# Kernel tuning notes

Measured on AMD Instinct MI355X. Metric: run time of the kernel, lower is better.

Reference implementation:

```python
import jax, jax.numpy as jnp
import numpy as np

B, T, C = 2, 2048, 2048
H, D = 16, 128  # num_heads, head_dim


def setup_inputs() -> dict:
    key = jax.random.key(0)
    ks = jax.random.split(key, 5)
    x = jax.random.normal(ks[0], (B, T, C), dtype=jnp.float32)
    # causal mask: mask==0 positions are filled with -inf
    mask = jnp.tril(jnp.ones((T, T), dtype=jnp.int32))[None, None, :, :]
    wq = jax.random.normal(ks[1], (C, C), dtype=jnp.float32) * (C ** -0.5)
    wk = jax.random.normal(ks[2], (C, C), dtype=jnp.float32) * (C ** -0.5)
    wv = jax.random.normal(ks[3], (C, C), dtype=jnp.float32) * (C ** -0.5)
    wo = jax.random.normal(ks[4], (C, C), dtype=jnp.float32) * (C ** -0.5)
    return {"x": x, "mask": mask, "wq": wq, "wk": wk, "wv": wv, "wo": wo}


def reference(x, mask, wq, wk, wv, wo):
    Bx, Tx, Cx = x.shape
    scale = D ** -0.5
    # torch Linear: y = x @ W.T (weights are [out, in])
    q = (x @ wq.T).reshape(Bx, Tx, H, D).transpose(0, 2, 1, 3)  # [B,H,T,D]
    k = (x @ wk.T).reshape(Bx, Tx, H, D).transpose(0, 2, 1, 3)
    v = (x @ wv.T).reshape(Bx, Tx, H, D).transpose(0, 2, 1, 3)
    scores = jnp.einsum("bhqd,bhkd->bhqk", q, k) * scale  # [B,H,T,T]
    scores = jnp.where(mask == 0, -jnp.inf, scores)
    attn = jax.nn.softmax(scores, axis=-1)
    out = jnp.einsum("bhqk,bhkd->bhqd", attn, v)  # [B,H,T,D]
    out = out.transpose(0, 2, 1, 3).reshape(Bx, Tx, Cx)
    return out @ wo.T
```

## Files before the change

### kernel.cpp

```cpp
#include <hip/hip_runtime.h>
#include <hip/hip_bf16.h>


#define BB 2
#define TT 2048
#define CC 2048
#define HH 16
#define DD 128
#define MM (BB*TT)
#define NQT (TT/64)
#define GNT (CC/64)

typedef __bf16 bf16x8 __attribute__((ext_vector_type(8)));
typedef __bf16 bf16x4 __attribute__((ext_vector_type(4)));
typedef float  f32x4  __attribute__((ext_vector_type(4)));

#define MFMA16(a, b, c) __builtin_amdgcn_mfma_f32_16x16x32_bf16((a), (b), (c), 0, 0, 0)

__device__ __forceinline__ void g2lds16(const void* g, void* l) {
    __builtin_amdgcn_global_load_lds(
        (const __attribute__((address_space(1))) void*)g,
        (__attribute__((address_space(3))) void*)l,
        16, 0, 0);
}

__global__ __launch_bounds__(256) void cvt_all(
    const float* __restrict__ x,  const float* __restrict__ wq,
    const float* __restrict__ wk, const float* __restrict__ wv,
    const float* __restrict__ wo, __bf16* __restrict__ out_base)
{
    const int idx = blockIdx.x * 256 + threadIdx.x;
    const float* in; int off;
    if (idx < (1 << 21)) { in = x; off = idx; }
    else {
        const int r = idx - (1 << 21);
        const int k = r >> 20;
        in  = (k == 0) ? wq : (k == 1) ? wk : (k == 2) ? wv : wo;
        off = r & ((1 << 20) - 1);
    }
    const float4 v = ((const float4*)in)[off];
    bf16x4 o;
    o.x = (__bf16)v.x; o.y = (__bf16)v.y;
    o.z = (__bf16)v.z; o.w = (__bf16)v.w;
    ((bf16x4*)out_base)[idx] = o;
}

template<int MODE>
__global__ __launch_bounds__(512, 2) void gemm_bt(
    const __bf16* __restrict__ A, const __bf16* __restrict__ Wt,
    void* __restrict__ out)
{
    __shared__ __align__(16) __bf16 As[3][256*64];
    __shared__ __align__(16) __bf16 Bs[3][2][128*32];

    const int tid = threadIdx.x;
    const int w   = tid >> 6, lane = tid & 63;
    const int wm  = w >> 1,  wn  = w & 1;
    const int lo  = lane & 15, hi = lane >> 4;
    const int xr  = (lo & 7) << 4;
    const int xb2 = ((lo >> 1) & 3) << 4;

    const int bid   = blockIdx.y * gridDim.x + blockIdx.x;
    const int xcd   = bid & 7, loc = bid >> 3;
    const int n0    = (2*xcd + (loc & 1)) * 128;
    const int m0    = (loc >> 1) * 256;

    const int ar   = tid >> 3, as_ = tid & 7;
    const int acol = ((as_ ^ (ar & 7)) << 3);
    const int br   = tid >> 2, bs_ = tid & 3;
    const int bcol = ((bs_ ^ ((br >> 1) & 3)) << 3);

    auto stageA3a = [&](int buf, int kt) {
        #pragma unroll
        for (int j = 0; j < 3; ++j)
            g2lds16(A + (size_t)(m0 + j*64 + ar)*CC + kt*64 + acol,
                    (char*)&As[buf][0] + j*8192 + w*1024);
    };
    auto stageA3b = [&](int buf, int kt) {
        g2lds16(A + (size_t)(m0 + 3*64 + ar)*CC + kt*64 + acol,
                (char*)&As[buf][0] + 3*8192 + w*1024);
        #pragma unroll
        for (int kh = 0; kh < 2; ++kh)
            g2lds16(Wt + (size_t)(n0 + br)*CC + kt*64 + kh*32 + bcol,
                    (char*)&Bs[buf][kh][0] + w*1024);
    };
    auto rdA = [&](bf16x8* af, int buf, int ks) {
        const char* base = (const char*)&As[buf][0];
        #pragma unroll
        for (int mf = 0; mf < 4; ++mf) {
            const int r = wm*64 + mf*16 + lo;
            af[mf] = *(const bf16x8*)(base + r*128 + ((ks*64 + hi*16) ^ xr));
        }
    };
    auto rdB = [&](bf16x8* bv, int buf, int ks) {
        const char* base = (const char*)&Bs[buf][ks][0];
        #pragma unroll
        for (int nf = 0; nf < 4; ++nf) {
            const int n = wn*64 + nf*16 + lo;
            bv[nf] = *(const bf16x8*)(base + n*64 + ((hi*16) ^ xb2));
        }
    };

    f32x4 acc[4][4] = {};

    stageA3a(0, 0); stageA3b(0, 0);
    stageA3a(1, 1); stageA3b(1, 1);
    asm volatile("s_waitcnt vmcnt(6)" ::: "memory");
    __builtin_amdgcn_s_barrier();

    int rb = 0;
    #pragma unroll 1
    for (int t = 0; t < GNT - 2; ++t) {
        const int sb = (rb == 0) ? 2 : rb - 1;
        {
            bf16x8 af[4], bv[4];
            rdA(af, rb, 0); rdB(bv, rb, 0);
            stageA3a(sb, t + 2);
            __builtin_amdgcn_s_barrier();
            __builtin_amdgcn_s_setprio(1);
            #pragma unroll
            for (int mf = 0; mf < 4; ++mf)
                #pragma unroll
                for (int nf = 0; nf < 4; ++nf)
                    acc[mf][nf] = MFMA16(af[mf], bv[nf], acc[mf][nf]);
            __builtin_amdgcn_s_setprio(0);
            __builtin_amdgcn_s_barrier();
        }
        {
            bf16x8 af[4], bv[4];
            rdA(af, rb, 1); rdB(bv, rb, 1);
            stageA3b(sb, t + 2);
            __builtin_amdgcn_s_barrier();
            __builtin_amdgcn_s_setprio(1);
            #pragma unroll
            for (int mf = 0; mf < 4; ++mf)
                #pragma unroll
                for (int nf = 0; nf < 4; ++nf)
                    acc[mf][nf] = MFMA16(af[mf], bv[nf], acc[mf][nf]);
            __builtin_amdgcn_s_setprio(0);
            asm volatile("s_waitcnt vmcnt(6)" ::: "memory");
            __builtin_amdgcn_s_barrier();
        }
        rb = (rb == 2) ? 0 : rb + 1;
    }
    {
        bf16x8 af[4], bv[4];
        rdA(af, rb, 0); rdB(bv, rb, 0);
        __builtin_amdgcn_s_barrier();
        #pragma unroll
        for (int mf = 0; mf < 4; ++mf)
            #pragma unroll
            for (int nf = 0; nf < 4; ++nf)
                acc[mf][nf] = MFMA16(af[mf], bv[nf], acc[mf][nf]);
        __builtin_amdgcn_s_barrier();
        rdA(af, rb, 1); rdB(bv, rb, 1);
        #pragma unroll
        for (int mf = 0; mf < 4; ++mf)
            #pragma unroll
            for (int nf = 0; nf < 4; ++nf)
                acc[mf][nf] = MFMA16(af[mf], bv[nf], acc[mf][nf]);
        asm volatile("s_waitcnt vmcnt(0)" ::: "memory");
        __builtin_amdgcn_s_barrier();
        rb = (rb == 2) ? 0 : rb + 1;
    }
    {
        bf16x8 af[4], bv[4];
        rdA(af, rb, 0); rdB(bv, rb, 0);
        #pragma unroll
        for (int mf = 0; mf < 4; ++mf)
            #pragma unroll
            for (int nf = 0; nf < 4; ++nf)
                acc[mf][nf] = MFMA16(af[mf], bv[nf], acc[mf][nf]);
        rdA(af, rb, 1); rdB(bv, rb, 1);
        #pragma unroll
        for (int mf = 0; mf < 4; ++mf)
            #pragma unroll
            for (int nf = 0; nf < 4; ++nf)
                acc[mf][nf] = MFMA16(af[mf], bv[nf], acc[mf][nf]);
    }

    #pragma unroll
    for (int mf = 0; mf < 4; ++mf) {
        #pragma unroll
        for (int nf = 0; nf < 4; ++nf) {
            #pragma unroll
            for (int r = 0; r < 4; ++r) {
                const int row = m0 + wm*64 + mf*16 + hi*4 + r;
                const int col = n0 + wn*64 + nf*16 + lo;
                const float v = acc[mf][nf][r];
                if (MODE == 0) {
                    const int b = row >> 11, t = row & (TT-1);
                    const int h = col >> 7,  d = col & (DD-1);
                    ((__bf16*)out)[(size_t)((b*HH + h)*TT + t)*DD + d] = (__bf16)v;
                } else if (MODE == 1) {
                    const int b = row >> 11, t = row & (TT-1);
                    const int h = col >> 7,  d = col & (DD-1);
                    ((__bf16*)out)[(size_t)((b*HH + h)*DD + d)*TT + t] = (__bf16)v;
                } else {
                    ((float*)out)[(size_t)row*CC + col] = v;
                }
            }
        }
    }
}

__global__ __launch_bounds__(256, 2) void attn_fwd(
    const __bf16* __restrict__ Q, const __bf16* __restrict__ K,
    const __bf16* __restrict__ Vt, __bf16* __restrict__ O)
{
    __shared__ __align__(16) __bf16 Ks[2][64*128];
    __shared__ __align__(16) __bf16 Vs[2][128*64];
    __shared__ __align__(16) __bf16 Ps[4][16*64];

    const int lid   = blockIdx.y * gridDim.x + blockIdx.x;
    const int bh    = lid & 31;
    const int pairx = lid >> 5;
    const int tid = threadIdx.x;
    const int w   = tid >> 6, lane = tid & 63;
    const int lo  = lane & 15, hi = lane >> 4;
    const int xr  = (lo & 7) << 4;

    const int krow_l  = lane >> 4;
    const int kcol_sw = ((lane & 15) << 4);
    const int vrow_l  = lane >> 3;
    const int vcol_sw = (((lane & 7) ^ (lane >> 3)) << 3);

    const size_t kbase = (size_t)bh * TT * DD;
    const size_t vbase = (size_t)bh * DD * TT;
    const int b = bh >> 4, h = bh & 15;
    const float SC = 0.12754613142f;

    auto stage = [&](int buf, int kv0) {
        #pragma unroll
        for (int i = 0; i < 4; ++i) {
            const int c = 4*w + i;
            {
                const int row = 4*c + krow_l;
                const int sw  = (kcol_sw ^ ((row & 7) << 4)) >> 1;
                g2lds16(K + kbase + (size_t)(kv0 + row)*DD + sw,
                        &Ks[buf][0] + c*512);
            }
            {
                const int row = 8*c + vrow_l;
                g2lds16(Vt + vbase + (size_t)row*TT + kv0 + vcol_sw,
                        &Vs[buf][0] + c*512);
            }
        }
    };

    #pragma unroll 1
    for (int half = 0; half < 2; ++half) {
        const int qt = half ? pairx : (NQT - 1 - pairx);
        const int q0 = qt * 64;

        const __bf16* Qbase = Q + (kbase + (size_t)(q0 + w*16 + lo) * DD);
        bf16x8 qf[4];
        #pragma unroll
        for (int kc = 0; kc < 4; ++kc)
            qf[kc] = *(const bf16x8*)(Qbase + kc*32 + hi*8);

        float mrow[4], lrow[4];
        #pragma unroll
        for (int r = 0; r < 4; ++r) { mrow[r] = -1e30f; lrow[r] = 0.f; }
        f32x4 oacc[8] = {};

        const int qg_base = q0 + w*16 + hi*4;
        const int ntiles  = qt + 1;

        stage(0, 0);
        __syncthreads();
        int cur = 0;

        for (int t = 0; t < ntiles; ++t) {
            const int kv0 = t*64;
            if (t + 1 < ntiles) stage(cur ^ 1, (t+1)*64);

            const char* Kb = (const char*)&Ks[cur][0];
            const char* Vb = (const char*)&Vs[cur][0];

            f32x4 s[4];
            __builtin_amdgcn_s_setprio(1);
            #pragma unroll
            for (int st = 0; st < 4; ++st) {
                f32x4 a = {};
                #pragma unroll
                for (int kc = 0; kc < 4; ++kc) {
                    const bf16x8 kf = *(const bf16x8*)(
                        Kb + (st*16 + lo)*256 + ((kc*64 + hi*16) ^ xr));
                    a = MFMA16(qf[kc], kf, a);
                }
                s[st] = a;
            }
            __builtin_amdgcn_s_setprio(0);

            float pmax[4];
            const bool diag = (t == ntiles - 1);
            #pragma unroll
            for (int r = 0; r < 4; ++r) {
                const int qg = qg_base + r;
                float mx = -1e30f;
                #pragma unroll
                for (int st = 0; st < 4; ++st) {
                    float v = s[st][r] * SC;
                    if (diag) {
                        const int kvg = kv0 + st*16 + lo;
                        v = (kvg > qg) ? -1e30f : v;
                    }
                    s[st][r] = v;
                    mx = fmaxf(mx, v);
                }
                #pragma unroll
                for (int msk = 1; msk < 16; msk <<= 1)
                    mx = fmaxf(mx, __shfl_xor(mx, msk, 64));
                pmax[r] = mx;
            }

            bool need = false;
            #pragma unroll
            for (int r = 0; r < 4; ++r)
                need = need || (pmax[r] > mrow[r] + 11.5f);
            if (__any(need)) {
                float rsc[4];
                #pragma unroll
                for (int r = 0; r < 4; ++r) {
                    const float mnew = fmaxf(mrow[r], pmax[r]);
                    rsc[r]  = __builtin_amdgcn_exp2f(mrow[r] - mnew);
                    mrow[r] = mnew;
                    lrow[r] *= rsc[r];
                }
                #pragma unroll
                for (int dc = 0; dc < 8; ++dc)
                    #pragma unroll
                    for (int r = 0; r < 4; ++r)
                        oacc[dc][r] *= rsc[r];
            }

            float psum[4];
            #pragma unroll
            for (int r = 0; r < 4; ++r) {
                float ps = 0.f;
                #pragma unroll
                for (int st = 0; st < 4; ++st) {
                    const float pv = __builtin_amdgcn_exp2f(s[st][r] - mrow[r]);
                    s[st][r] = pv;
                    ps += pv;
                }
                psum[r] = ps;
            }
            #pragma unroll
            for (int r = 0; r < 4; ++r) {
                #pragma unroll
                for (int msk = 1; msk < 16; msk <<= 1)
                    psum[r] += __shfl_xor(psum[r], msk, 64);
                lrow[r] += psum[r];
            }

            char* Pw = (char*)&Ps[w][0];
            #pragma unroll
            for (int st = 0; st < 4; ++st)
                #pragma unroll
                for (int r = 0; r < 4; ++r) {
                    const int row = hi*4 + r;
                    *(__bf16*)(Pw + row*128 + (((st*16 + lo)*2) ^ ((row & 7) << 4)))
                        = (__bf16)s[st][r];
                }

            __builtin_amdgcn_s_setprio(1);
            #pragma unroll
            for (int kc2 = 0; kc2 < 2; ++kc2) {
                const bf16x8 pf = *(const bf16x8*)(
                    Pw + lo*128 + ((kc2*64 + hi*16) ^ xr));
                #pragma unroll
                for (int dc = 0; dc < 8; ++dc) {
                    const bf16x8 vf = *(const bf16x8*)(
                        Vb + (dc*16 + lo)*128 + ((kc2*64 + hi*16) ^ xr));
                    oacc[dc] = MFMA16(pf, vf, oacc[dc]);
                }
            }
            __builtin_amdgcn_s_setprio(0);

            __syncthreads();
            cur ^= 1;
        }

        #pragma unroll
        for (int r = 0; r < 4; ++r) {
            const float inv = 1.f / lrow[r];
            const int qg = qg_base + r;
            #pragma unroll
            for (int dc = 0; dc < 8; ++dc) {
                const int d = dc*16 + lo;
                O[(size_t)(b*TT + qg)*CC + h*DD + d] = (__bf16)(oacc[dc][r] * inv);
            }
        }
    }
}

extern "C" void kernel_launch(void* const* d_in, const int* in_sizes, int n_in,
                              void* d_out, int out_size, void* d_ws, size_t ws_size,
                              hipStream_t stream) {
    const float* x  = (const float*)d_in[0];
    const float* wq = (const float*)d_in[2];
    const float* wk = (const float*)d_in[3];
    const float* wv = (const float*)d_in[4];
    const float* wo = (const float*)d_in[5];

    char* p = (char*)d_ws;
    __bf16* xb  = (__bf16*)p; p += (size_t)MM*CC*2;
    __bf16* wqb = (__bf16*)p; p += (size_t)CC*CC*2;
    __bf16* wkb = (__bf16*)p; p += (size_t)CC*CC*2;
    __bf16* wvb = (__bf16*)p; p += (size_t)CC*CC*2;
    __bf16* wob = (__bf16*)p; p += (size_t)CC*CC*2;
    __bf16* Qb  = (__bf16*)p; p += (size_t)MM*CC*2;
    __bf16* Kb  = (__bf16*)p; p += (size_t)MM*CC*2;
    __bf16* Vtb = (__bf16*)p; p += (size_t)MM*CC*2;
    __bf16* AOb = xb;

    cvt_all<<<24576, 256, 0, stream>>>(x, wq, wk, wv, wo, xb);

    const dim3 gg(CC/128, MM/256);
    gemm_bt<0><<<gg, 512, 0, stream>>>(xb, wqb, Qb);
    gemm_bt<0><<<gg, 512, 0, stream>>>(xb, wkb, Kb);
    gemm_bt<1><<<gg, 512, 0, stream>>>(xb, wvb, Vtb);

    attn_fwd<<<dim3(NQT/2, BB*HH), 256, 0, stream>>>(Qb, Kb, Vtb, AOb);

    gemm_bt<2><<<gg, 512, 0, stream>>>(AOb, wob, (void*)d_out);
}
```

Baseline: 248.8 us.

## Halve attention KV tile to 32, raise occupancy, one query tile per block

```diff
diff --git a/kernel.cpp b/kernel.cpp
--- a/kernel.cpp
+++ b/kernel.cpp
@@ -10,6 +10,7 @@
 #define MM (BB*TT)
 #define NQT (TT/64)
 #define GNT (CC/64)
+#define KVB 32
 
 typedef __bf16 bf16x8 __attribute__((ext_vector_type(8)));
 typedef __bf16 bf16x4 __attribute__((ext_vector_type(4)));
@@ -204,26 +205,24 @@
     }
 }
 
-__global__ __launch_bounds__(256, 2) void attn_fwd(
+__global__ __launch_bounds__(256, 4) void attn_fwd(
     const __bf16* __restrict__ Q, const __bf16* __restrict__ K,
     const __bf16* __restrict__ Vt, __bf16* __restrict__ O)
 {
-    __shared__ __align__(16) __bf16 Ks[2][64*128];
-    __shared__ __align__(16) __bf16 Vs[2][128*64];
-    __shared__ __align__(16) __bf16 Ps[4][16*64];
-
-    const int lid   = blockIdx.y * gridDim.x + blockIdx.x;
-    const int bh    = lid & 31;
-    const int pairx = lid >> 5;
+    __shared__ __align__(16) __bf16 Ks[2][KVB*128];
+    __shared__ __align__(16) __bf16 Vs[2][128*KVB];
+    __shared__ __align__(16) __bf16 Ps[4][16*KVB];
+
+    const int bh = blockIdx.x;
+    const int aq = blockIdx.y & 7, bq = blockIdx.y >> 3;
+    const int qt = 8*bq + ((bq & 1) ? 7 - aq : aq);
+    const int q0 = qt * 64;
+
     const int tid = threadIdx.x;
     const int w   = tid >> 6, lane = tid & 63;
     const int lo  = lane & 15, hi = lane >> 4;
     const int xr  = (lo & 7) << 4;
-
-    const int krow_l  = lane >> 4;
-    const int kcol_sw = ((lane & 15) << 4);
-    const int vrow_l  = lane >> 3;
-    const int vcol_sw = (((lane & 7) ^ (lane >> 3)) << 3);
+    const int pvx = ((lo & 3) ^ ((lo >> 2) & 3)) << 4;
 
     const size_t kbase = (size_t)bh * TT * DD;
     const size_t vbase = (size_t)bh * DD * TT;
@@ -232,166 +231,161 @@
 
     auto stage = [&](int buf, int kv0) {
         #pragma unroll
-        for (int i = 0; i < 4; ++i) {
-            const int c = 4*w + i;
+        for (int i = 0; i < 2; ++i) {
+            const int c = 2*w + i;
             {
-                const int row = 4*c + krow_l;
-                const int sw  = (kcol_sw ^ ((row & 7) << 4)) >> 1;
+                const int row = 4*c + (lane >> 4);
+                const int sw  = ((((lane & 15) << 4) ^ ((row & 7) << 4)) >> 1);
                 g2lds16(K + kbase + (size_t)(kv0 + row)*DD + sw,
                         &Ks[buf][0] + c*512);
             }
             {
-                const int row = 8*c + vrow_l;
-                g2lds16(Vt + vbase + (size_t)row*TT + kv0 + vcol_sw,
+                const int rl  = lane >> 2;
+                const int row = 16*c + rl;
+                const int el  = ((((lane & 3) ^ (rl & 3) ^ ((rl >> 2) & 3))) << 3);
+                g2lds16(Vt + vbase + (size_t)row*TT + kv0 + el,
                         &Vs[buf][0] + c*512);
             }
         }
     };
 
-    #pragma unroll 1
-    for (int half = 0; half < 2; ++half) {
-        const int qt = half ? pairx : (NQT - 1 - pairx);
-        const int q0 = qt * 64;
-
-        const __bf16* Qbase = Q + (kbase + (size_t)(q0 + w*16 + lo) * DD);
-        bf16x8 qf[4];
-        #pragma unroll
-        for (int kc = 0; kc < 4; ++kc)
-            qf[kc] = *(const bf16x8*)(Qbase + kc*32 + hi*8);
-
-        float mrow[4], lrow[4];
-        #pragma unroll
-        for (int r = 0; r < 4; ++r) { mrow[r] = -1e30f; lrow[r] = 0.f; }
-        f32x4 oacc[8] = {};
-
-        const int qg_base = q0 + w*16 + hi*4;
-        const int ntiles  = qt + 1;
-
-        stage(0, 0);
+    const __bf16* Qbase = Q + (kbase + (size_t)(q0 + w*16 + lo) * DD);
+    bf16x8 qf[4];
+    #pragma unroll
+    for (int kc = 0; kc < 4; ++kc)
+        qf[kc] = *(const bf16x8*)(Qbase + kc*32 + hi*8);
+
+    float mrow[4], lrow[4];
+    #pragma unroll
+    for (int r = 0; r < 4; ++r) { mrow[r] = -1e30f; lrow[r] = 0.f; }
+    f32x4 oacc[8] = {};
+
+    const int qg_base = q0 + w*16 + hi*4;
+    const int ntiles  = 2*(qt + 1);
+
+    stage(0, 0);
+    __syncthreads();
+    int cur = 0;
+
+    for (int t = 0; t < ntiles; ++t) {
+        const int kv0 = t*KVB;
+        if (t + 1 < ntiles) stage(cur ^ 1, (t+1)*KVB);
+
+        const char* Kb = (const char*)&Ks[cur][0];
+        const char* Vb = (const char*)&Vs[cur][0];
+
+        f32x4 s[2];
+        __builtin_amdgcn_s_setprio(1);
+        #pragma unroll
+        for (int st = 0; st < 2; ++st) {
+            f32x4 a = {};
+            #pragma unroll
+            for (int kc = 0; kc < 4; ++kc) {
+                const bf16x8 kf = *(const bf16x8*)(
+                    Kb + (st*16 + lo)*256 + ((kc*64 + hi*16) ^ xr));
+                a = MFMA16(qf[kc], kf, a);
+            }
+            s[st] = a;
+        }
+        __builtin_amdgcn_s_setprio(0);
+
+        float pmax[4];
+        const bool diag = (t >= ntiles - 2);
+        #pragma unroll
+        for (int r = 0; r < 4; ++r) {
+            const int qg = qg_base + r;
+            float mx = -1e30f;
+            #pragma unroll
+            for (int st = 0; st < 2; ++st) {
+                float v = s[st][r] * SC;
+                if (diag) {
+                    const int kvg = kv0 + st*16 + lo;
+                    v = (kvg > qg) ? -1e30f : v;
+                }
+                s[st][r] = v;
+                mx = fmaxf(mx, v);
+            }
+            #pragma unroll
+            for (int msk = 1; msk < 16; msk <<= 1)
+                mx = fmaxf(mx, __shfl_xor(mx, msk, 64));
+            pmax[r] = mx;
+        }
+
+        bool need = false;
+        #pragma unroll
+        for (int r = 0; r < 4; ++r)
+            need = need || (pmax[r] > mrow[r] + 11.5f);
+        if (__any(need)) {
+            float rsc[4];
+            #pragma unroll
+            for (int r = 0; r < 4; ++r) {
+                const float mnew = fmaxf(mrow[r], pmax[r]);
+                rsc[r]  = __builtin_amdgcn_exp2f(mrow[r] - mnew);
+                mrow[r] = mnew;
+                lrow[r] *= rsc[r];
+            }
+            #pragma unroll
+            for (int dc = 0; dc < 8; ++dc)
+                #pragma unroll
+                for (int r = 0; r < 4; ++r)
+                    oacc[dc][r] *= rsc[r];
+        }
+
+        float psum[4];
+        #pragma unroll
+        for (int r = 0; r < 4; ++r) {
+            float ps = 0.f;
+            #pragma unroll
+            for (int st = 0; st < 2; ++st) {
+                const float pv = __builtin_amdgcn_exp2f(s[st][r] - mrow[r]);
+                s[st][r] = pv;
+                ps += pv;
+            }
+            psum[r] = ps;
+        }
+        #pragma unroll
+        for (int r = 0; r < 4; ++r) {
+            #pragma unroll
+            for (int msk = 1; msk < 16; msk <<= 1)
+                psum[r] += __shfl_xor(psum[r], msk, 64);
+            lrow[r] += psum[r];
+        }
+
+        char* Pw = (char*)&Ps[w][0];
+        #pragma unroll
+        for (int st = 0; st < 2; ++st)
+            #pragma unroll
+            for (int r = 0; r < 4; ++r) {
+                const int row = hi*4 + r;
+                const int sw  = (((row & 3) ^ ((row >> 2) & 3)) << 4);
+                *(__bf16*)(Pw + row*64 + (((st*16 + lo)*2) ^ sw))
+                    = (__bf16)s[st][r];
+            }
+
+        __builtin_amdgcn_s_setprio(1);
+        {
+            const bf16x8 pf = *(const bf16x8*)(Pw + lo*64 + ((hi*16) ^ pvx));
+            #pragma unroll
+            for (int dc = 0; dc < 8; ++dc) {
+                const bf16x8 vf = *(const bf16x8*)(
+                    Vb + (dc*16 + lo)*64 + ((hi*16) ^ pvx));
+                oacc[dc] = MFMA16(pf, vf, oacc[dc]);
+            }
+        }
+        __builtin_amdgcn_s_setprio(0);
+
         __syncthreads();
-        int cur = 0;
-
-        for (int t = 0; t < ntiles; ++t) {
-            const int kv0 = t*64;
-            if (t + 1 < ntiles) stage(cur ^ 1, (t+1)*64);
-
-            const char* Kb = (const char*)&Ks[cur][0];
-            const char* Vb = (const char*)&Vs[cur][0];
-
-            f32x4 s[4];
-            __builtin_amdgcn_s_setprio(1);
-            #pragma unroll
-            for (int st = 0; st < 4; ++st) {
-                f32x4 a = {};
-                #pragma unroll
-                for (int kc = 0; kc < 4; ++kc) {
-                    const bf16x8 kf = *(const bf16x8*)(
-                        Kb + (st*16 + lo)*256 + ((kc*64 + hi*16) ^ xr));
-                    a = MFMA16(qf[kc], kf, a);
-                }
-                s[st] = a;
-            }
-            __builtin_amdgcn_s_setprio(0);
-
-            float pmax[4];
-            const bool diag = (t == ntiles - 1);
-            #pragma unroll
-            for (int r = 0; r < 4; ++r) {
-                const int qg = qg_base + r;
-                float mx = -1e30f;
-                #pragma unroll
-                for (int st = 0; st < 4; ++st) {
-                    float v = s[st][r] * SC;
-                    if (diag) {
-                        const int kvg = kv0 + st*16 + lo;
-                        v = (kvg > qg) ? -1e30f : v;
-                    }
-                    s[st][r] = v;
-                    mx = fmaxf(mx, v);
-                }
-                #pragma unroll
-                for (int msk = 1; msk < 16; msk <<= 1)
-                    mx = fmaxf(mx, __shfl_xor(mx, msk, 64));
-                pmax[r] = mx;
-            }
-
-            bool need = false;
-            #pragma unroll
-            for (int r = 0; r < 4; ++r)
-                need = need || (pmax[r] > mrow[r] + 11.5f);
-            if (__any(need)) {
-                float rsc[4];
-                #pragma unroll
-                for (int r = 0; r < 4; ++r) {
-                    const float mnew = fmaxf(mrow[r], pmax[r]);
-                    rsc[r]  = __builtin_amdgcn_exp2f(mrow[r] - mnew);
-                    mrow[r] = mnew;
-                    lrow[r] *= rsc[r];
-                }
-                #pragma unroll
-                for (int dc = 0; dc < 8; ++dc)
-                    #pragma unroll
-                    for (int r = 0; r < 4; ++r)
-                        oacc[dc][r] *= rsc[r];
-            }
-
-            float psum[4];
-            #pragma unroll
-            for (int r = 0; r < 4; ++r) {
-                float ps = 0.f;
-                #pragma unroll
-                for (int st = 0; st < 4; ++st) {
-                    const float pv = __builtin_amdgcn_exp2f(s[st][r] - mrow[r]);
-                    s[st][r] = pv;
-                    ps += pv;
-                }
-                psum[r] = ps;
-            }
-            #pragma unroll
-            for (int r = 0; r < 4; ++r) {
-                #pragma unroll
-                for (int msk = 1; msk < 16; msk <<= 1)
-                    psum[r] += __shfl_xor(psum[r], msk, 64);
-                lrow[r] += psum[r];
-            }
-
-            char* Pw = (char*)&Ps[w][0];
-            #pragma unroll
-            for (int st = 0; st < 4; ++st)
-                #pragma unroll
-                for (int r = 0; r < 4; ++r) {
-                    const int row = hi*4 + r;
-                    *(__bf16*)(Pw + row*128 + (((st*16 + lo)*2) ^ ((row & 7) << 4)))
-                        = (__bf16)s[st][r];
-                }
-
-            __builtin_amdgcn_s_setprio(1);
-            #pragma unroll
-            for (int kc2 = 0; kc2 < 2; ++kc2) {
-                const bf16x8 pf = *(const bf16x8*)(
-                    Pw + lo*128 + ((kc2*64 + hi*16) ^ xr));
-                #pragma unroll
-                for (int dc = 0; dc < 8; ++dc) {
-                    const bf16x8 vf = *(const bf16x8*)(
-                        Vb + (dc*16 + lo)*128 + ((kc2*64 + hi*16) ^ xr));
-                    oacc[dc] = MFMA16(pf, vf, oacc[dc]);
-                }
-            }
-            __builtin_amdgcn_s_setprio(0);
-
-            __syncthreads();
-            cur ^= 1;
-        }
-
-        #pragma unroll
-        for (int r = 0; r < 4; ++r) {
-            const float inv = 1.f / lrow[r];
-            const int qg = qg_base + r;
-            #pragma unroll
-            for (int dc = 0; dc < 8; ++dc) {
-                const int d = dc*16 + lo;
-                O[(size_t)(b*TT + qg)*CC + h*DD + d] = (__bf16)(oacc[dc][r] * inv);
-            }
+        cur ^= 1;
+    }
+
+    #pragma unroll
+    for (int r = 0; r < 4; ++r) {
+        const float inv = 1.f / lrow[r];
+        const int qg = qg_base + r;
+        #pragma unroll
+        for (int dc = 0; dc < 8; ++dc) {
+            const int d = dc*16 + lo;
+            O[(size_t)(b*TT + qg)*CC + h*DD + d] = (__bf16)(oacc[dc][r] * inv);
         }
     }
 }
@@ -423,7 +417,7 @@
     gemm_bt<0><<<gg, 512, 0, stream>>>(xb, wkb, Kb);
     gemm_bt<1><<<gg, 512, 0, stream>>>(xb, wvb, Vtb);
 
-    attn_fwd<<<dim3(NQT/2, BB*HH), 256, 0, stream>>>(Qb, Kb, Vtb, AOb);
+    attn_fwd<<<dim3(BB*HH, NQT), 256, 0, stream>>>(Qb, Kb, Vtb, AOb);
 
     gemm_bt<2><<<gg, 512, 0, stream>>>(AOb, wob, (void*)d_out);
 }
```

New measurement: 292.8 us. +17.7%, slower.

## Single-buffer attention LDS, one query tile per block, raise occupancy

Applied to the files above, without the earlier changes.

```diff
diff --git a/kernel.cpp b/kernel.cpp
--- a/kernel.cpp
+++ b/kernel.cpp
@@ -204,17 +204,18 @@
     }
 }
 
-__global__ __launch_bounds__(256, 2) void attn_fwd(
+__global__ __launch_bounds__(256, 4) void attn_fwd(
     const __bf16* __restrict__ Q, const __bf16* __restrict__ K,
     const __bf16* __restrict__ Vt, __bf16* __restrict__ O)
 {
-    __shared__ __align__(16) __bf16 Ks[2][64*128];
-    __shared__ __align__(16) __bf16 Vs[2][128*64];
+    __shared__ __align__(16) __bf16 Ks[64*128];
+    __shared__ __align__(16) __bf16 Vs[128*64];
     __shared__ __align__(16) __bf16 Ps[4][16*64];
 
-    const int lid   = blockIdx.y * gridDim.x + blockIdx.x;
-    const int bh    = lid & 31;
-    const int pairx = lid >> 5;
+    const int bh = blockIdx.x;
+    const int qt = (NQT - 1) - (int)blockIdx.y;
+    const int q0 = qt * 64;
+
     const int tid = threadIdx.x;
     const int w   = tid >> 6, lane = tid & 63;
     const int lo  = lane & 15, hi = lane >> 4;
@@ -230,7 +231,7 @@
     const int b = bh >> 4, h = bh & 15;
     const float SC = 0.12754613142f;
 
-    auto stage = [&](int buf, int kv0) {
+    auto stage = [&](int kv0) {
         #pragma unroll
         for (int i = 0; i < 4; ++i) {
             const int c = 4*w + i;
@@ -238,160 +239,150 @@
                 const int row = 4*c + krow_l;
                 const int sw  = (kcol_sw ^ ((row & 7) << 4)) >> 1;
                 g2lds16(K + kbase + (size_t)(kv0 + row)*DD + sw,
-                        &Ks[buf][0] + c*512);
+                        Ks + c*512);
             }
             {
                 const int row = 8*c + vrow_l;
                 g2lds16(Vt + vbase + (size_t)row*TT + kv0 + vcol_sw,
-                        &Vs[buf][0] + c*512);
+                        Vs + c*512);
             }
         }
     };
 
-    #pragma unroll 1
-    for (int half = 0; half < 2; ++half) {
-        const int qt = half ? pairx : (NQT - 1 - pairx);
-        const int q0 = qt * 64;
-
-        const __bf16* Qbase = Q + (kbase + (size_t)(q0 + w*16 + lo) * DD);
-        bf16x8 qf[4];
-        #pragma unroll
-        for (int kc = 0; kc < 4; ++kc)
-            qf[kc] = *(const bf16x8*)(Qbase + kc*32 + hi*8);
-
-        float mrow[4], lrow[4];
-        #pragma unroll
-        for (int r = 0; r < 4; ++r) { mrow[r] = -1e30f; lrow[r] = 0.f; }
-        f32x4 oacc[8] = {};
-
-        const int qg_base = q0 + w*16 + hi*4;
-        const int ntiles  = qt + 1;
-
-        stage(0, 0);
+    const __bf16* Qbase = Q + (kbase + (size_t)(q0 + w*16 + lo) * DD);
+    bf16x8 qf[4];
+    #pragma unroll
+    for (int kc = 0; kc < 4; ++kc)
+        qf[kc] = *(const bf16x8*)(Qbase + kc*32 + hi*8);
+
+    float mrow[4], lrow[4];
+    #pragma unroll
+    for (int r = 0; r < 4; ++r) { mrow[r] = -1e30f; lrow[r] = 0.f; }
+    f32x4 oacc[8] = {};
+
+    const int qg_base = q0 + w*16 + hi*4;
+    const int ntiles  = qt + 1;
+
+    for (int t = 0; t < ntiles; ++t) {
+        const int kv0 = t*64;
+        stage(kv0);
         __syncthreads();
-        int cur = 0;
-
-        for (int t = 0; t < ntiles; ++t) {
-            const int kv0 = t*64;
-            if (t + 1 < ntiles) stage(cur ^ 1, (t+1)*64);
-
-            const char* Kb = (const char*)&Ks[cur][0];
-            const char* Vb = (const char*)&Vs[cur][0];
-
-            f32x4 s[4];
-            __builtin_amdgcn_s_setprio(1);
+
+        const char* Kb = (const char*)Ks;
+        const char* Vb = (const char*)Vs;
+
+        f32x4 s[4];
+        __builtin_amdgcn_s_setprio(1);
+        #pragma unroll
+        for (int st = 0; st < 4; ++st) {
+            f32x4 a = {};
+            #pragma unroll
+            for (int kc = 0; kc < 4; ++kc) {
+                const bf16x8 kf = *(const bf16x8*)(
+                    Kb + (st*16 + lo)*256 + ((kc*64 + hi*16) ^ xr));
+                a = MFMA16(qf[kc], kf, a);
+            }
+            s[st] = a;
+        }
+        __builtin_amdgcn_s_setprio(0);
+
+        float pmax[4];
+        const bool diag = (t == ntiles - 1);
+        #pragma unroll
+        for (int r = 0; r < 4; ++r) {
+            const int qg = qg_base + r;
+            float mx = -1e30f;
             #pragma unroll
             for (int st = 0; st < 4; ++st) {
-                f32x4 a = {};
+                float v = s[st][r] * SC;
+                if (diag) {
+                    const int kvg = kv0 + st*16 + lo;
+                    v = (kvg > qg) ? -1e30f : v;
+                }
+                s[st][r] = v;
+                mx = fmaxf(mx, v);
+            }
+            #pragma unroll
+            for (int msk = 1; msk < 16; msk <<= 1)
+                mx = fmaxf(mx, __shfl_xor(mx, msk, 64));
+            pmax[r] = mx;
+        }
+
+        bool need = false;
+        #pragma unroll
+        for (int r = 0; r < 4; ++r)
+            need = need || (pmax[r] > mrow[r] + 11.5f);
+        if (__any(need)) {
+            float rsc[4];
+            #pragma unroll
+            for (int r = 0; r < 4; ++r) {
+                const float mnew = fmaxf(mrow[r], pmax[r]);
+                rsc[r]  = __builtin_amdgcn_exp2f(mrow[r] - mnew);
+                mrow[r] = mnew;
+                lrow[r] *= rsc[r];
+            }
+            #pragma unroll
+            for (int dc = 0; dc < 8; ++dc)
                 #pragma unroll
-                for (int kc = 0; kc < 4; ++kc) {
-                    const bf16x8 kf = *(const bf16x8*)(
-                        Kb + (st*16 + lo)*256 + ((kc*64 + hi*16) ^ xr));
-                    a = MFMA16(qf[kc], kf, a);
-                }
-                s[st] = a;
-            }
-            __builtin_amdgcn_s_setprio(0);
-
-            float pmax[4];
-            const bool diag = (t == ntiles - 1);
+                for (int r = 0; r < 4; ++r)
+                    oacc[dc][r] *= rsc[r];
+        }
+
+        float psum[4];
+        #pragma unroll
+        for (int r = 0; r < 4; ++r) {
+            float ps = 0.f;
+            #pragma unroll
+            for (int st = 0; st < 4; ++st) {
+                const float pv = __builtin_amdgcn_exp2f(s[st][r] - mrow[r]);
+                s[st][r] = pv;
+                ps += pv;
+            }
+            psum[r] = ps;
+        }
+        #pragma unroll
+        for (int r = 0; r < 4; ++r) {
+            #pragma unroll
+            for (int msk = 1; msk < 16; msk <<= 1)
+                psum[r] += __shfl_xor(psum[r], msk, 64);
+            lrow[r] += psum[r];
+        }
+
+        char* Pw = (char*)&Ps[w][0];
+        #pragma unroll
+        for (int st = 0; st < 4; ++st)
             #pragma unroll
             for (int r = 0; r < 4; ++r) {
-                const int qg = qg_base + r;
-                float mx = -1e30f;
-                #pragma unroll
-                for (int st = 0; st < 4; ++st) {
-                    float v = s[st][r] * SC;
-                    if (diag) {
-                        const int kvg = kv0 + st*16 + lo;
-                        v = (kvg > qg) ? -1e30f : v;
-                    }
-                    s[st][r] = v;
-                    mx = fmaxf(mx, v);
-                }
-                #pragma unroll
-                for (int msk = 1; msk < 16; msk <<= 1)
-                    mx = fmaxf(mx, __shfl_xor(mx, msk, 64));
-                pmax[r] = mx;
-            }
-
-            bool need = false;
-            #pragma unroll
-            for (int r = 0; r < 4; ++r)
-                need = need || (pmax[r] > mrow[r] + 11.5f);
-            if (__any(need)) {
-                float rsc[4];
-                #pragma unroll
-                for (int r = 0; r < 4; ++r) {
-                    const float mnew = fmaxf(mrow[r], pmax[r]);
-                    rsc[r]  = __builtin_amdgcn_exp2f(mrow[r] - mnew);
-                    mrow[r] = mnew;
-                    lrow[r] *= rsc[r];
-                }
-                #pragma unroll
-                for (int dc = 0; dc < 8; ++dc)
-                    #pragma unroll
-                    for (int r = 0; r < 4; ++r)
-                        oacc[dc][r] *= rsc[r];
-            }
-
-            float psum[4];
-            #pragma unroll
-            for (int r = 0; r < 4; ++r) {
-                float ps = 0.f;
-                #pragma unroll
-                for (int st = 0; st < 4; ++st) {
-                    const float pv = __builtin_amdgcn_exp2f(s[st][r] - mrow[r]);
-                    s[st][r] = pv;
-                    ps += pv;
-                }
-                psum[r] = ps;
-            }
-            #pragma unroll
-            for (int r = 0; r < 4; ++r) {
-                #pragma unroll
-                for (int msk = 1; msk < 16; msk <<= 1)
-                    psum[r] += __shfl_xor(psum[r], msk, 64);
-                lrow[r] += psum[r];
-            }
-
-            char* Pw = (char*)&Ps[w][0];
-            #pragma unroll
-            for (int st = 0; st < 4; ++st)
-                #pragma unroll
-                for (int r = 0; r < 4; ++r) {
-                    const int row = hi*4 + r;
-                    *(__bf16*)(Pw + row*128 + (((st*16 + lo)*2) ^ ((row & 7) << 4)))
-                        = (__bf16)s[st][r];
-                }
-
-            __builtin_amdgcn_s_setprio(1);
-            #pragma unroll
-            for (int kc2 = 0; kc2 < 2; ++kc2) {
-                const bf16x8 pf = *(const bf16x8*)(
-                    Pw + lo*128 + ((kc2*64 + hi*16) ^ xr));
-                #pragma unroll
-                for (int dc = 0; dc < 8; ++dc) {
-                    const bf16x8 vf = *(const bf16x8*)(
-                        Vb + (dc*16 + lo)*128 + ((kc2*64 + hi*16) ^ xr));
-                    oacc[dc] = MFMA16(pf, vf, oacc[dc]);
-                }
-            }
-            __builtin_amdgcn_s_setprio(0);
-
-            __syncthreads();
-            cur ^= 1;
-        }
-
-        #pragma unroll
-        for (int r = 0; r < 4; ++r) {
-            const float inv = 1.f / lrow[r];
-            const int qg = qg_base + r;
+                const int row = hi*4 + r;
+                *(__bf16*)(Pw + row*128 + (((st*16 + lo)*2) ^ ((row & 7) << 4)))
+                    = (__bf16)s[st][r];
+            }
+
+        __builtin_amdgcn_s_setprio(1);
+        #pragma unroll
+        for (int kc2 = 0; kc2 < 2; ++kc2) {
+            const bf16x8 pf = *(const bf16x8*)(
+                Pw + lo*128 + ((kc2*64 + hi*16) ^ xr));
             #pragma unroll
             for (int dc = 0; dc < 8; ++dc) {
-                const int d = dc*16 + lo;
-                O[(size_t)(b*TT + qg)*CC + h*DD + d] = (__bf16)(oacc[dc][r] * inv);
-            }
+                const bf16x8 vf = *(const bf16x8*)(
+                    Vb + (dc*16 + lo)*128 + ((kc2*64 + hi*16) ^ xr));
+                oacc[dc] = MFMA16(pf, vf, oacc[dc]);
+            }
+        }
+        __builtin_amdgcn_s_setprio(0);
+
+        __syncthreads();
+    }
+
+    #pragma unroll
+    for (int r = 0; r < 4; ++r) {
+        const float inv = 1.f / lrow[r];
+        const int qg = qg_base + r;
+        #pragma unroll
+        for (int dc = 0; dc < 8; ++dc) {
+            const int d = dc*16 + lo;
+            O[(size_t)(b*TT + qg)*CC + h*DD + d] = (__bf16)(oacc[dc][r] * inv);
         }
     }
 }
@@ -423,7 +414,7 @@
     gemm_bt<0><<<gg, 512, 0, stream>>>(xb, wkb, Kb);
     gemm_bt<1><<<gg, 512, 0, stream>>>(xb, wvb, Vtb);
 
-    attn_fwd<<<dim3(NQT/2, BB*HH), 256, 0, stream>>>(Qb, Kb, Vtb, AOb);
+    attn_fwd<<<dim3(BB*HH, NQT), 256, 0, stream>>>(Qb, Kb, Vtb, AOb);
 
     gemm_bt<2><<<gg, 512, 0, stream>>>(AOb, wob, (void*)d_out);
 }
```

Result: slower. 279.7 us (+12.4%).
